# Optimization experiments

Measured on AMD Instinct MI355X. Metric: run time of the kernel, lower is better.

Reference implementation:

```python
import jax, jax.numpy as jnp
import numpy as np

B, N, C_X, D_MODEL, D_OUT, S = 32, 4096, 1, 64, 1, 2
D_IN = C_X + D_MODEL  # 65, channels entering graph_conv


def setup_inputs() -> dict:
    key = jax.random.key(0)
    ks = jax.random.split(key, 8)
    x = jax.random.normal(ks[0], (B, C_X, N), dtype=jnp.float32)
    h = jax.random.normal(ks[1], (B, D_MODEL, N), dtype=jnp.float32)
    # stacked support matrices (fwd/bwd normalized adjacency), used as a list of supports
    adj = jax.random.uniform(ks[2], (S, N, N), dtype=jnp.float32) / N
    # graph_conv.mlp : Conv2d(S*D_IN -> D_MODEL, 1x1)
    W_mlp = jax.random.normal(ks[3], (D_MODEL, S * D_IN), dtype=jnp.float32) / np.sqrt(S * D_IN)
    b_mlp = jnp.zeros((D_MODEL,), jnp.float32)
    # lin_out : Conv1d(2*D_MODEL -> D_MODEL, k=1)
    W_lin = jax.random.normal(ks[4], (D_MODEL, 2 * D_MODEL), dtype=jnp.float32) / np.sqrt(2 * D_MODEL)
    b_lin = jnp.zeros((D_MODEL,), jnp.float32)
    # read_out : Conv1d(2*D_MODEL -> D_OUT, k=1)
    W_read = jax.random.normal(ks[5], (D_OUT, 2 * D_MODEL), dtype=jnp.float32) / np.sqrt(2 * D_MODEL)
    b_read = jnp.zeros((D_OUT,), jnp.float32)
    prelu_a = jnp.array(0.25, jnp.float32)  # nn.PReLU() default: single shared slope
    return {"x": x, "h": h, "adj": adj, "W_mlp": W_mlp, "b_mlp": b_mlp,
            "W_lin": W_lin, "b_lin": b_lin, "W_read": W_read, "b_read": b_read,
            "prelu_a": prelu_a}


def conv1x1(W, b, x):
    # x: [B, C_in, N] -> [B, C_out, N]
    return jnp.einsum('oc,bcn->bon', W, x) + b[None, :, None]


def reference(x, h, adj, W_mlp, b_mlp, W_lin, b_lin, W_read, b_read, prelu_a):
    # x: [B, C_X, N], h: [B, D_MODEL, N], adj: [S, N, N]
    x_in = jnp.concatenate([x, h], axis=1)  # [B, D_IN, N]
    # SpatialConvOrderK (order=1, include_self=False):
    # out[b,c,w] per support s = sum_v x_in[b,c,v] * adj[s,w,v]
    hops = jnp.einsum('bcv,swv->bscw', x_in, adj)  # [B, S, D_IN, N]
    feats = hops.reshape(B, S * D_IN, N)           # channel-cat over supports
    out = conv1x1(W_mlp, b_mlp, feats)             # [B, D_MODEL, N]
    out = jnp.concatenate([out, h], axis=1)        # [B, 2*D_MODEL, N]
    out = conv1x1(W_lin, b_lin, out)               # [B, D_MODEL, N]
    out = jnp.where(out >= 0, out, prelu_a * out)  # PReLU
    out = jnp.concatenate([out, h], axis=1)        # [B, 2*D_MODEL, N]
    return (conv1x1(W_read, b_read, out), out)
```

## Files before the change

kernel.cpp:

```cpp
#include <hip/hip_runtime.h>
#include <cstdint>

#define N_NODES 4096
#define DM 64
#define K_DIM 8192
#define M_DIM 2048

typedef uint8_t u8;
using i32x8   = __attribute__((ext_vector_type(8))) int;
using floatx4 = __attribute__((ext_vector_type(4))) float;

#define GLOAD_LDS16(gp, lp)                                                     \
  __builtin_amdgcn_global_load_lds(                                             \
      reinterpret_cast<const __attribute__((address_space(1))) void*>(          \
          reinterpret_cast<uintptr_t>(gp)),                                     \
      reinterpret_cast<__attribute__((address_space(3))) void*>(                \
          (uint32_t)reinterpret_cast<uintptr_t>(lp)),                           \
      16, 0, 0)

__device__ inline int pk_fp8x4(float f0, float f1, float f2, float f3) {
  int r = __builtin_amdgcn_cvt_pk_fp8_f32(f0, f1, 0, false);
  r     = __builtin_amdgcn_cvt_pk_fp8_f32(f2, f3, r, true);
  return r;
}

__global__ __launch_bounds__(256) void k_prep(const float* __restrict__ adj,
                                              u8* __restrict__ BT8,
                                              const float* __restrict__ x,
                                              const float* __restrict__ h,
                                              const float* __restrict__ Wmlp,
                                              u8* __restrict__ A8) {
  __shared__ __align__(16) float Ws[DM * 68];
  uint32_t bi = blockIdx.x;
  if (bi >= 1024u) {
    const uint32_t lane = threadIdx.x & 63u;
    uint32_t gw = (bi - 1024u) * 4u + (threadIdx.x >> 6);
    for (uint32_t sc = gw; sc < 16384u; sc += 8192u) {
      const float4* src = reinterpret_cast<const float4*>(adj) + (size_t)sc * 512u + lane;
      float4 f[8];
#pragma unroll
      for (int q = 0; q < 8; ++q) f[q] = src[(size_t)q * 64];
      uint32_t row = sc >> 1;
      uint32_t s = row >> 12, w = row & 4095u;
      u8* dst = BT8 + (size_t)w * K_DIM + s * N_NODES + (sc & 1u) * 2048u + lane * 4u;
#pragma unroll
      for (int q = 0; q < 8; ++q) {
        int p = pk_fp8x4(f[q].x * 4096.f, f[q].y * 4096.f, f[q].z * 4096.f, f[q].w * 4096.f);
        *reinterpret_cast<int*>(dst + q * 256) = p;
      }
    }
    return;
  }
  uint32_t b2 = bi;
  uint32_t v0 = (b2 & 15u) * 256u;
  uint32_t s  = (b2 >> 4) & 1u;
  uint32_t b  = b2 >> 5;
  for (uint32_t t = threadIdx.x; t < DM * 68; t += 256) {
    uint32_t d = t / 68u, c = t % 68u;
    Ws[t] = (c < 65u) ? Wmlp[d * 130u + s * 65u + c] : 0.f;
  }
  __syncthreads();

  const uint32_t tv = threadIdx.x & 63u;
  const uint32_t td = threadIdx.x >> 6;
  const uint32_t v  = v0 + tv * 4u;

  float acc[16][4];
#pragma unroll
  for (int d = 0; d < 16; ++d)
#pragma unroll
    for (int k = 0; k < 4; ++k) acc[d][k] = 0.f;

  for (int c0 = 0; c0 < 64; c0 += 4) {
    float4 in4[4];
#pragma unroll
    for (int j = 0; j < 4; ++j) {
      int c = c0 + j;
      const float* src = (c == 0) ? (x + (size_t)b * N_NODES + v)
                                  : (h + ((size_t)b * DM + (c - 1)) * N_NODES + v);
      in4[j] = *reinterpret_cast<const float4*>(src);
    }
#pragma unroll
    for (int d = 0; d < 16; ++d) {
      const float4 w4 = *reinterpret_cast<const float4*>(&Ws[(td * 16 + d) * 68 + c0]);
      acc[d][0] += w4.x * in4[0].x + w4.y * in4[1].x + w4.z * in4[2].x + w4.w * in4[3].x;
      acc[d][1] += w4.x * in4[0].y + w4.y * in4[1].y + w4.z * in4[2].y + w4.w * in4[3].y;
      acc[d][2] += w4.x * in4[0].z + w4.y * in4[1].z + w4.z * in4[2].z + w4.w * in4[3].z;
      acc[d][3] += w4.x * in4[0].w + w4.y * in4[1].w + w4.z * in4[2].w + w4.w * in4[3].w;
    }
  }
  {
    float4 in4 = *reinterpret_cast<const float4*>(h + ((size_t)b * DM + 63) * N_NODES + v);
#pragma unroll
    for (int d = 0; d < 16; ++d) {
      float w = Ws[(td * 16 + d) * 68 + 64];
      acc[d][0] += w * in4.x; acc[d][1] += w * in4.y;
      acc[d][2] += w * in4.z; acc[d][3] += w * in4.w;
    }
  }
#pragma unroll
  for (int d = 0; d < 16; ++d) {
    int p = pk_fp8x4(acc[d][0], acc[d][1], acc[d][2], acc[d][3]);
    *reinterpret_cast<int*>(A8 + (size_t)(b * DM + td * 16 + d) * K_DIM + s * N_NODES + v) = p;
  }
}

__global__ void k_gemm(const u8* __restrict__ A, const u8* __restrict__ BT,
                       const float* __restrict__ h,
                       const float* __restrict__ bmlp, const float* __restrict__ Wlin,
                       const float* __restrict__ blin, const float* __restrict__ Wread,
                       const float* __restrict__ bread, const float* __restrict__ pa,
                       float* __restrict__ out0, float* __restrict__ out1) {
  __shared__ __align__(32) char smem[64 * 132 * 4];
  __shared__ __align__(16) float sbm[DM], sbl[DM], sWr[128];
  __shared__ __align__(16) float psum[8 * 128];

  u8 (*As)[128][32] = reinterpret_cast<u8(*)[128][32]>(smem);
  u8 (*Bs)[128][32] = reinterpret_cast<u8(*)[128][32]>(smem + 16384);
  float (*gco)[132] = reinterpret_cast<float(*)[132]>(smem);

  const int tid  = threadIdx.x;
  const int lane = tid & 63;
  const int wave = tid >> 6;
  const int wr = wave >> 1, wc = wave & 1;

  uint32_t bi  = blockIdx.x;
  uint32_t bi2 = (bi & 7u) * 64u + (bi >> 3);
  const int xt = bi2 & 31, yt = bi2 >> 5;
  const int m0 = yt * 128, n0 = xt * 128;
  const int b0 = yt * 2;

  if (tid < DM)  { sbm[tid] = bmlp[tid]; sbl[tid] = blin[tid]; }
  if (tid < 128) sWr[tid] = Wread[tid];
  const float aP = pa[0];
  const float br = bread[0];

  const int srow  = lane >> 1;
  const int shalf = (lane & 1) * 16;
  const u8* Ag = A  + (size_t)(m0 + wave * 32 + srow) * K_DIM + shalf;
  const u8* Bg = BT + (size_t)(n0 + wave * 32 + srow) * K_DIM + shalf;
  u8* AsB[4]; u8* BsB[4];
#pragma unroll
  for (int q = 0; q < 4; ++q) { AsB[q] = &As[q][wave * 32][0]; BsB[q] = &Bs[q][wave * 32][0]; }

  floatx4 acc[4][4];
#pragma unroll
  for (int i = 0; i < 4; ++i)
#pragma unroll
    for (int j = 0; j < 4; ++j) acc[i][j] = (floatx4){0.f, 0.f, 0.f, 0.f};

  const int fm = lane & 15;
  const int fq = lane >> 4;
  const int SC1 = 0x7F7F7F7F;

  for (int k0 = 0; k0 < 8192; k0 += 128) {
#pragma unroll
    for (int q = 0; q < 4; ++q) GLOAD_LDS16(Ag + k0 + q * 32, AsB[q]);
#pragma unroll
    for (int q = 0; q < 4; ++q) GLOAD_LDS16(Bg + k0 + q * 32, BsB[q]);
    __syncthreads();

    i32x8 af[4], bfr[4];
#pragma unroll
    for (int i = 0; i < 4; ++i)
      af[i] = *reinterpret_cast<const i32x8*>(&As[fq][wr * 64 + i * 16 + fm][0]);
#pragma unroll
    for (int j = 0; j < 4; ++j)
      bfr[j] = *reinterpret_cast<const i32x8*>(&Bs[fq][wc * 64 + j * 16 + fm][0]);
#pragma unroll
    for (int i = 0; i < 4; ++i)
#pragma unroll
      for (int j = 0; j < 4; ++j)
        acc[i][j] = __builtin_amdgcn_mfma_scale_f32_16x16x128_f8f6f4(
            af[i], bfr[j], acc[i][j], 0, 0, 0, SC1, 0, SC1);
    __syncthreads();
  }

  const float KS = 1.0f / 4096.0f;
  const int cr = (lane >> 4) * 4;
  const int cc = lane & 15;
  const int dsub = wave * 2 + (lane >> 5);
  const int ncol = (lane & 31) * 4;
  const float* Wl0 = Wlin + (size_t)(dsub * 8) * 128;

  for (int p = 0; p < 2; ++p) {
    if (wr == p) {
#pragma unroll
      for (int i = 0; i < 4; ++i)
#pragma unroll
        for (int j = 0; j < 4; ++j) {
#pragma unroll
          for (int r = 0; r < 4; ++r) {
            int d = i * 16 + cr + r;
            gco[d][wc * 64 + j * 16 + cc] = acc[i][j][r] * KS + sbm[d];
          }
        }
    }
    __syncthreads();

    const int b = b0 + p;
    float z[8][4];
#pragma unroll
    for (int dd = 0; dd < 8; ++dd) {
      float bl = sbl[dsub * 8 + dd];
#pragma unroll
      for (int k = 0; k < 4; ++k) z[dd][k] = bl;
    }

    for (int k0 = 0; k0 < 64; k0 += 4) {
      float4 g[4];
#pragma unroll
      for (int j = 0; j < 4; ++j)
        g[j] = *reinterpret_cast<const float4*>(&gco[k0 + j][ncol]);
#pragma unroll
      for (int dd = 0; dd < 8; ++dd) {
        const float4 w4 = *reinterpret_cast<const float4*>(Wl0 + (size_t)dd * 128 + k0);
        z[dd][0] += w4.x * g[0].x + w4.y * g[1].x + w4.z * g[2].x + w4.w * g[3].x;
        z[dd][1] += w4.x * g[0].y + w4.y * g[1].y + w4.z * g[2].y + w4.w * g[3].y;
        z[dd][2] += w4.x * g[0].z + w4.y * g[1].z + w4.z * g[2].z + w4.w * g[3].z;
        z[dd][3] += w4.x * g[0].w + w4.y * g[1].w + w4.z * g[2].w + w4.w * g[3].w;
      }
    }

    const float* hb = h + (size_t)b * DM * N_NODES + n0 + ncol;
    float* o1b = out1 + (size_t)b * 128 * N_NODES + n0 + ncol;
    float hs[4] = {0.f, 0.f, 0.f, 0.f};
    for (int k0 = 0; k0 < 64; k0 += 4) {
      float4 hv[4];
#pragma unroll
      for (int j = 0; j < 4; ++j)
        hv[j] = *reinterpret_cast<const float4*>(hb + (size_t)(k0 + j) * N_NODES);
#pragma unroll
      for (int dd = 0; dd < 8; ++dd) {
        const float4 w4 = *reinterpret_cast<const float4*>(Wl0 + (size_t)dd * 128 + 64 + k0);
        z[dd][0] += w4.x * hv[0].x + w4.y * hv[1].x + w4.z * hv[2].x + w4.w * hv[3].x;
        z[dd][1] += w4.x * hv[0].y + w4.y * hv[1].y + w4.z * hv[2].y + w4.w * hv[3].y;
        z[dd][2] += w4.x * hv[0].z + w4.y * hv[1].z + w4.z * hv[2].z + w4.w * hv[3].z;
        z[dd][3] += w4.x * hv[0].w + w4.y * hv[1].w + w4.z * hv[2].w + w4.w * hv[3].w;
      }
      if (dsub == 0) {
#pragma unroll
        for (int j = 0; j < 4; ++j) {
          *reinterpret_cast<float4*>(o1b + (size_t)(64 + k0 + j) * N_NODES) = hv[j];
          float w = sWr[64 + k0 + j];
          hs[0] += w * hv[j].x; hs[1] += w * hv[j].y;
          hs[2] += w * hv[j].z; hs[3] += w * hv[j].w;
        }
      }
    }

    float rp[4] = {0.f, 0.f, 0.f, 0.f};
#pragma unroll
    for (int dd = 0; dd < 8; ++dd) {
      int dp = dsub * 8 + dd;
      float4 o2;
      o2.x = z[dd][0] >= 0.f ? z[dd][0] : aP * z[dd][0];
      o2.y = z[dd][1] >= 0.f ? z[dd][1] : aP * z[dd][1];
      o2.z = z[dd][2] >= 0.f ? z[dd][2] : aP * z[dd][2];
      o2.w = z[dd][3] >= 0.f ? z[dd][3] : aP * z[dd][3];
      *reinterpret_cast<float4*>(o1b + (size_t)dp * N_NODES) = o2;
      float w = sWr[dp];
      rp[0] += w * o2.x; rp[1] += w * o2.y; rp[2] += w * o2.z; rp[3] += w * o2.w;
    }
    if (dsub == 0) {
      rp[0] += hs[0]; rp[1] += hs[1]; rp[2] += hs[2]; rp[3] += hs[3];
    }
    {
      float4 rv; rv.x = rp[0]; rv.y = rp[1]; rv.z = rp[2]; rv.w = rp[3];
      *reinterpret_cast<float4*>(&psum[dsub * 128 + ncol]) = rv;
    }
    __syncthreads();
    if (wave == 0 && lane < 32) {
      float s0[4];
#pragma unroll
      for (int k = 0; k < 4; ++k) {
        float s = br;
#pragma unroll
        for (int ds = 0; ds < 8; ++ds) s += psum[ds * 128 + ncol + k];
        s0[k] = s;
      }
      float4 ov; ov.x = s0[0]; ov.y = s0[1]; ov.z = s0[2]; ov.w = s0[3];
      *reinterpret_cast<float4*>(out0 + (size_t)b * N_NODES + n0 + ncol) = ov;
    }
    __syncthreads();
  }
}

extern "C" void kernel_launch(void* const* d_in, const int* in_sizes, int n_in,
                              void* d_out, int out_size, void* d_ws, size_t ws_size,
                              hipStream_t stream) {
  const float* x     = (const float*)d_in[0];
  const float* h     = (const float*)d_in[1];
  const float* adj   = (const float*)d_in[2];
  const float* Wmlp  = (const float*)d_in[3];
  const float* bmlp  = (const float*)d_in[4];
  const float* Wlin  = (const float*)d_in[5];
  const float* blin  = (const float*)d_in[6];
  const float* Wread = (const float*)d_in[7];
  const float* bread = (const float*)d_in[8];
  const float* pa    = (const float*)d_in[9];

  char* ws = (char*)d_ws;
  u8*    Abuf  = (u8*)ws;
  u8*    BTbuf = (u8*)(ws + (16ull << 20));
  float* out0 = (float*)d_out;
  float* out1 = out0 + 131072;

  hipLaunchKernelGGL(k_prep, dim3(3072), dim3(256), 0, stream,
                     adj, BTbuf, x, h, Wmlp, Abuf);
  hipLaunchKernelGGL(k_gemm, dim3(512),  dim3(256), 0, stream,
                     Abuf, BTbuf, h, bmlp, Wlin, blin, Wread, bread, pa, out0, out1);
}
```

Before: 449.8 us.

## Use 512-thread GEMM blocks with split load roles and XCD-aware tile mapping

```diff
diff --git a/kernel.cpp b/kernel.cpp
--- a/kernel.cpp
+++ b/kernel.cpp
@@ -105,15 +105,16 @@
   }
 }
 
-__global__ void k_gemm(const u8* __restrict__ A, const u8* __restrict__ BT,
-                       const float* __restrict__ h,
-                       const float* __restrict__ bmlp, const float* __restrict__ Wlin,
-                       const float* __restrict__ blin, const float* __restrict__ Wread,
-                       const float* __restrict__ bread, const float* __restrict__ pa,
-                       float* __restrict__ out0, float* __restrict__ out1) {
+__global__ __launch_bounds__(512, 4) void k_gemm(
+    const u8* __restrict__ A, const u8* __restrict__ BT,
+    const float* __restrict__ h,
+    const float* __restrict__ bmlp, const float* __restrict__ Wlin,
+    const float* __restrict__ blin, const float* __restrict__ Wread,
+    const float* __restrict__ bread, const float* __restrict__ pa,
+    float* __restrict__ out0, float* __restrict__ out1) {
   __shared__ __align__(32) char smem[64 * 132 * 4];
   __shared__ __align__(16) float sbm[DM], sbl[DM], sWr[128];
-  __shared__ __align__(16) float psum[8 * 128];
+  __shared__ __align__(16) float psum[16 * 128];
 
   u8 (*As)[128][32] = reinterpret_cast<u8(*)[128][32]>(smem);
   u8 (*Bs)[128][32] = reinterpret_cast<u8(*)[128][32]>(smem + 16384);
@@ -125,27 +126,31 @@
   const int wr = wave >> 1, wc = wave & 1;
 
   uint32_t bi  = blockIdx.x;
-  uint32_t bi2 = (bi & 7u) * 64u + (bi >> 3);
-  const int xt = bi2 & 31, yt = bi2 >> 5;
+  uint32_t xcd = bi & 7u, idx = bi >> 3;
+  const int yt = (int)((xcd & 1u) * 8u + (idx & 7u));
+  const int xt = (int)((xcd >> 1) * 8u + (idx >> 3));
   const int m0 = yt * 128, n0 = xt * 128;
   const int b0 = yt * 2;
 
   if (tid < DM)  { sbm[tid] = bmlp[tid]; sbl[tid] = blin[tid]; }
-  if (tid < 128) sWr[tid] = Wread[tid];
+  if (tid >= 64 && tid < 192) sWr[tid - 64] = Wread[tid - 64];
   const float aP = pa[0];
   const float br = bread[0];
 
   const int srow  = lane >> 1;
   const int shalf = (lane & 1) * 16;
-  const u8* Ag = A  + (size_t)(m0 + wave * 32 + srow) * K_DIM + shalf;
-  const u8* Bg = BT + (size_t)(n0 + wave * 32 + srow) * K_DIM + shalf;
-  u8* AsB[4]; u8* BsB[4];
-#pragma unroll
-  for (int q = 0; q < 4; ++q) { AsB[q] = &As[q][wave * 32][0]; BsB[q] = &Bs[q][wave * 32][0]; }
-
-  floatx4 acc[4][4];
-#pragma unroll
-  for (int i = 0; i < 4; ++i)
+  const bool isA  = wave < 4;
+  const int wrow  = (wave & 3) * 32;
+  const u8* Sg = (isA ? A + (size_t)(m0 + wrow + srow) * K_DIM
+                      : BT + (size_t)(n0 + wrow + srow) * K_DIM) + shalf;
+  u8* SdB[4];
+#pragma unroll
+  for (int q = 0; q < 4; ++q)
+    SdB[q] = isA ? &As[q][wrow][0] : &Bs[q][wrow][0];
+
+  floatx4 acc[2][4];
+#pragma unroll
+  for (int i = 0; i < 2; ++i)
 #pragma unroll
     for (int j = 0; j < 4; ++j) acc[i][j] = (floatx4){0.f, 0.f, 0.f, 0.f};
 
@@ -155,20 +160,18 @@
 
   for (int k0 = 0; k0 < 8192; k0 += 128) {
 #pragma unroll
-    for (int q = 0; q < 4; ++q) GLOAD_LDS16(Ag + k0 + q * 32, AsB[q]);
-#pragma unroll
-    for (int q = 0; q < 4; ++q) GLOAD_LDS16(Bg + k0 + q * 32, BsB[q]);
-    __syncthreads();
-
-    i32x8 af[4], bfr[4];
-#pragma unroll
-    for (int i = 0; i < 4; ++i)
-      af[i] = *reinterpret_cast<const i32x8*>(&As[fq][wr * 64 + i * 16 + fm][0]);
+    for (int q = 0; q < 4; ++q) GLOAD_LDS16(Sg + k0 + q * 32, SdB[q]);
+    __syncthreads();
+
+    i32x8 af[2], bfr[4];
+#pragma unroll
+    for (int i = 0; i < 2; ++i)
+      af[i] = *reinterpret_cast<const i32x8*>(&As[fq][wr * 32 + i * 16 + fm][0]);
 #pragma unroll
     for (int j = 0; j < 4; ++j)
       bfr[j] = *reinterpret_cast<const i32x8*>(&Bs[fq][wc * 64 + j * 16 + fm][0]);
 #pragma unroll
-    for (int i = 0; i < 4; ++i)
+    for (int i = 0; i < 2; ++i)
 #pragma unroll
       for (int j = 0; j < 4; ++j)
         acc[i][j] = __builtin_amdgcn_mfma_scale_f32_16x16x128_f8f6f4(
@@ -179,19 +182,19 @@
   const float KS = 1.0f / 4096.0f;
   const int cr = (lane >> 4) * 4;
   const int cc = lane & 15;
-  const int dsub = wave * 2 + (lane >> 5);
-  const int ncol = (lane & 31) * 4;
-  const float* Wl0 = Wlin + (size_t)(dsub * 8) * 128;
+  const int dsub = tid >> 5;
+  const int ncol = (tid & 31) * 4;
+  const float* Wl0 = Wlin + (size_t)(dsub * 4) * 128;
 
   for (int p = 0; p < 2; ++p) {
-    if (wr == p) {
-#pragma unroll
-      for (int i = 0; i < 4; ++i)
+    if ((wr >> 1) == p) {
+#pragma unroll
+      for (int i = 0; i < 2; ++i)
 #pragma unroll
         for (int j = 0; j < 4; ++j) {
 #pragma unroll
           for (int r = 0; r < 4; ++r) {
-            int d = i * 16 + cr + r;
+            int d = (wr & 1) * 32 + i * 16 + cr + r;
             gco[d][wc * 64 + j * 16 + cc] = acc[i][j][r] * KS + sbm[d];
           }
         }
@@ -199,10 +202,10 @@
     __syncthreads();
 
     const int b = b0 + p;
-    float z[8][4];
-#pragma unroll
-    for (int dd = 0; dd < 8; ++dd) {
-      float bl = sbl[dsub * 8 + dd];
+    float z[4][4];
+#pragma unroll
+    for (int dd = 0; dd < 4; ++dd) {
+      float bl = sbl[dsub * 4 + dd];
 #pragma unroll
       for (int k = 0; k < 4; ++k) z[dd][k] = bl;
     }
@@ -213,7 +216,7 @@
       for (int j = 0; j < 4; ++j)
         g[j] = *reinterpret_cast<const float4*>(&gco[k0 + j][ncol]);
 #pragma unroll
-      for (int dd = 0; dd < 8; ++dd) {
+      for (int dd = 0; dd < 4; ++dd) {
         const float4 w4 = *reinterpret_cast<const float4*>(Wl0 + (size_t)dd * 128 + k0);
         z[dd][0] += w4.x * g[0].x + w4.y * g[1].x + w4.z * g[2].x + w4.w * g[3].x;
         z[dd][1] += w4.x * g[0].y + w4.y * g[1].y + w4.z * g[2].y + w4.w * g[3].y;
@@ -231,7 +234,7 @@
       for (int j = 0; j < 4; ++j)
         hv[j] = *reinterpret_cast<const float4*>(hb + (size_t)(k0 + j) * N_NODES);
 #pragma unroll
-      for (int dd = 0; dd < 8; ++dd) {
+      for (int dd = 0; dd < 4; ++dd) {
         const float4 w4 = *reinterpret_cast<const float4*>(Wl0 + (size_t)dd * 128 + 64 + k0);
         z[dd][0] += w4.x * hv[0].x + w4.y * hv[1].x + w4.z * hv[2].x + w4.w * hv[3].x;
         z[dd][1] += w4.x * hv[0].y + w4.y * hv[1].y + w4.z * hv[2].y + w4.w * hv[3].y;
@@ -251,8 +254,8 @@
 
     float rp[4] = {0.f, 0.f, 0.f, 0.f};
 #pragma unroll
-    for (int dd = 0; dd < 8; ++dd) {
-      int dp = dsub * 8 + dd;
+    for (int dd = 0; dd < 4; ++dd) {
+      int dp = dsub * 4 + dd;
       float4 o2;
       o2.x = z[dd][0] >= 0.f ? z[dd][0] : aP * z[dd][0];
       o2.y = z[dd][1] >= 0.f ? z[dd][1] : aP * z[dd][1];
@@ -270,13 +273,13 @@
       *reinterpret_cast<float4*>(&psum[dsub * 128 + ncol]) = rv;
     }
     __syncthreads();
-    if (wave == 0 && lane < 32) {
+    if (tid < 32) {
       float s0[4];
 #pragma unroll
       for (int k = 0; k < 4; ++k) {
         float s = br;
 #pragma unroll
-        for (int ds = 0; ds < 8; ++ds) s += psum[ds * 128 + ncol + k];
+        for (int ds = 0; ds < 16; ++ds) s += psum[ds * 128 + ncol + k];
         s0[k] = s;
       }
       float4 ov; ov.x = s0[0]; ov.y = s0[1]; ov.z = s0[2]; ov.w = s0[3];
@@ -308,6 +311,6 @@
 
   hipLaunchKernelGGL(k_prep, dim3(3072), dim3(256), 0, stream,
                      adj, BTbuf, x, h, Wmlp, Abuf);
-  hipLaunchKernelGGL(k_gemm, dim3(512),  dim3(256), 0, stream,
+  hipLaunchKernelGGL(k_gemm, dim3(512),  dim3(512), 0, stream,
                      Abuf, BTbuf, h, bmlp, Wlin, blin, Wread, bread, pa, out0, out1);
 }
```

Measured after the change: 975.5 us. +116.9%, slower.

## Load FP8 MFMA fragments directly from global into registers with double buffering

Applied to the files above, without the earlier changes.

```diff
diff --git a/kernel.cpp b/kernel.cpp
--- a/kernel.cpp
+++ b/kernel.cpp
@@ -9,14 +9,6 @@
 typedef uint8_t u8;
 using i32x8   = __attribute__((ext_vector_type(8))) int;
 using floatx4 = __attribute__((ext_vector_type(4))) float;
-
-#define GLOAD_LDS16(gp, lp)                                                     \
-  __builtin_amdgcn_global_load_lds(                                             \
-      reinterpret_cast<const __attribute__((address_space(1))) void*>(          \
-          reinterpret_cast<uintptr_t>(gp)),                                     \
-      reinterpret_cast<__attribute__((address_space(3))) void*>(                \
-          (uint32_t)reinterpret_cast<uintptr_t>(lp)),                           \
-      16, 0, 0)
 
 __device__ inline int pk_fp8x4(float f0, float f1, float f2, float f3) {
   int r = __builtin_amdgcn_cvt_pk_fp8_f32(f0, f1, 0, false);
@@ -105,19 +97,17 @@
   }
 }
 
-__global__ void k_gemm(const u8* __restrict__ A, const u8* __restrict__ BT,
-                       const float* __restrict__ h,
-                       const float* __restrict__ bmlp, const float* __restrict__ Wlin,
-                       const float* __restrict__ blin, const float* __restrict__ Wread,
-                       const float* __restrict__ bread, const float* __restrict__ pa,
-                       float* __restrict__ out0, float* __restrict__ out1) {
-  __shared__ __align__(32) char smem[64 * 132 * 4];
+__global__ __launch_bounds__(256, 2) void k_gemm(
+    const u8* __restrict__ A, const u8* __restrict__ BT,
+    const float* __restrict__ h,
+    const float* __restrict__ bmlp, const float* __restrict__ Wlin,
+    const float* __restrict__ blin, const float* __restrict__ Wread,
+    const float* __restrict__ bread, const float* __restrict__ pa,
+    float* __restrict__ out0, float* __restrict__ out1) {
+  __shared__ __align__(16) float gco[64][132];
+  __shared__ __align__(16) float sW[DM * 132];
   __shared__ __align__(16) float sbm[DM], sbl[DM], sWr[128];
   __shared__ __align__(16) float psum[8 * 128];
-
-  u8 (*As)[128][32] = reinterpret_cast<u8(*)[128][32]>(smem);
-  u8 (*Bs)[128][32] = reinterpret_cast<u8(*)[128][32]>(smem + 16384);
-  float (*gco)[132] = reinterpret_cast<float(*)[132]>(smem);
 
   const int tid  = threadIdx.x;
   const int lane = tid & 63;
@@ -130,58 +120,72 @@
   const int m0 = yt * 128, n0 = xt * 128;
   const int b0 = yt * 2;
 
+  for (int t = tid; t < DM * 128; t += 256) {
+    int d = t >> 7, c = t & 127;
+    sW[d * 132 + c] = Wlin[t];
+  }
   if (tid < DM)  { sbm[tid] = bmlp[tid]; sbl[tid] = blin[tid]; }
   if (tid < 128) sWr[tid] = Wread[tid];
   const float aP = pa[0];
   const float br = bread[0];
 
-  const int srow  = lane >> 1;
-  const int shalf = (lane & 1) * 16;
-  const u8* Ag = A  + (size_t)(m0 + wave * 32 + srow) * K_DIM + shalf;
-  const u8* Bg = BT + (size_t)(n0 + wave * 32 + srow) * K_DIM + shalf;
-  u8* AsB[4]; u8* BsB[4];
-#pragma unroll
-  for (int q = 0; q < 4; ++q) { AsB[q] = &As[q][wave * 32][0]; BsB[q] = &Bs[q][wave * 32][0]; }
-
-  floatx4 acc[4][4];
-#pragma unroll
-  for (int i = 0; i < 4; ++i)
-#pragma unroll
-    for (int j = 0; j < 4; ++j) acc[i][j] = (floatx4){0.f, 0.f, 0.f, 0.f};
-
   const int fm = lane & 15;
   const int fq = lane >> 4;
+  const u8* Ab = A  + (size_t)(m0 + wr * 64 + fm) * K_DIM + fq * 32;
+  const u8* Bb = BT + (size_t)(n0 + wc * 64 + fm) * K_DIM + fq * 32;
+
+  floatx4 acc[4][4];
+#pragma unroll
+  for (int i = 0; i < 4; ++i)
+#pragma unroll
+    for (int j = 0; j < 4; ++j) acc[i][j] = (floatx4){0.f, 0.f, 0.f, 0.f};
+
   const int SC1 = 0x7F7F7F7F;
 
-  for (int k0 = 0; k0 < 8192; k0 += 128) {
-#pragma unroll
-    for (int q = 0; q < 4; ++q) GLOAD_LDS16(Ag + k0 + q * 32, AsB[q]);
-#pragma unroll
-    for (int q = 0; q < 4; ++q) GLOAD_LDS16(Bg + k0 + q * 32, BsB[q]);
-    __syncthreads();
-
-    i32x8 af[4], bfr[4];
+  i32x8 a0[4], b0v[4], a1[4], b1[4];
+#pragma unroll
+  for (int i = 0; i < 4; ++i)
+    a0[i] = *reinterpret_cast<const i32x8*>(Ab + (size_t)i * 16 * K_DIM);
+#pragma unroll
+  for (int j = 0; j < 4; ++j)
+    b0v[j] = *reinterpret_cast<const i32x8*>(Bb + (size_t)j * 16 * K_DIM);
+
+  for (int k0 = 0; k0 < 8192; k0 += 256) {
 #pragma unroll
     for (int i = 0; i < 4; ++i)
-      af[i] = *reinterpret_cast<const i32x8*>(&As[fq][wr * 64 + i * 16 + fm][0]);
+      a1[i] = *reinterpret_cast<const i32x8*>(Ab + (size_t)i * 16 * K_DIM + k0 + 128);
 #pragma unroll
     for (int j = 0; j < 4; ++j)
-      bfr[j] = *reinterpret_cast<const i32x8*>(&Bs[fq][wc * 64 + j * 16 + fm][0]);
+      b1[j] = *reinterpret_cast<const i32x8*>(Bb + (size_t)j * 16 * K_DIM + k0 + 128);
 #pragma unroll
     for (int i = 0; i < 4; ++i)
 #pragma unroll
       for (int j = 0; j < 4; ++j)
         acc[i][j] = __builtin_amdgcn_mfma_scale_f32_16x16x128_f8f6f4(
-            af[i], bfr[j], acc[i][j], 0, 0, 0, SC1, 0, SC1);
-    __syncthreads();
-  }
+            a0[i], b0v[j], acc[i][j], 0, 0, 0, SC1, 0, SC1);
+    if (k0 + 256 < 8192) {
+#pragma unroll
+      for (int i = 0; i < 4; ++i)
+        a0[i] = *reinterpret_cast<const i32x8*>(Ab + (size_t)i * 16 * K_DIM + k0 + 256);
+#pragma unroll
+      for (int j = 0; j < 4; ++j)
+        b0v[j] = *reinterpret_cast<const i32x8*>(Bb + (size_t)j * 16 * K_DIM + k0 + 256);
+    }
+#pragma unroll
+    for (int i = 0; i < 4; ++i)
+#pragma unroll
+      for (int j = 0; j < 4; ++j)
+        acc[i][j] = __builtin_amdgcn_mfma_scale_f32_16x16x128_f8f6f4(
+            a1[i], b1[j], acc[i][j], 0, 0, 0, SC1, 0, SC1);
+  }
+
+  __syncthreads();
 
   const float KS = 1.0f / 4096.0f;
   const int cr = (lane >> 4) * 4;
   const int cc = lane & 15;
   const int dsub = wave * 2 + (lane >> 5);
   const int ncol = (lane & 31) * 4;
-  const float* Wl0 = Wlin + (size_t)(dsub * 8) * 128;
 
   for (int p = 0; p < 2; ++p) {
     if (wr == p) {
@@ -214,7 +218,7 @@
         g[j] = *reinterpret_cast<const float4*>(&gco[k0 + j][ncol]);
 #pragma unroll
       for (int dd = 0; dd < 8; ++dd) {
-        const float4 w4 = *reinterpret_cast<const float4*>(Wl0 + (size_t)dd * 128 + k0);
+        const float4 w4 = *reinterpret_cast<const float4*>(&sW[(dsub * 8 + dd) * 132 + k0]);
         z[dd][0] += w4.x * g[0].x + w4.y * g[1].x + w4.z * g[2].x + w4.w * g[3].x;
         z[dd][1] += w4.x * g[0].y + w4.y * g[1].y + w4.z * g[2].y + w4.w * g[3].y;
         z[dd][2] += w4.x * g[0].z + w4.y * g[1].z + w4.z * g[2].z + w4.w * g[3].z;
@@ -232,7 +236,7 @@
         hv[j] = *reinterpret_cast<const float4*>(hb + (size_t)(k0 + j) * N_NODES);
 #pragma unroll
       for (int dd = 0; dd < 8; ++dd) {
-        const float4 w4 = *reinterpret_cast<const float4*>(Wl0 + (size_t)dd * 128 + 64 + k0);
+        const float4 w4 = *reinterpret_cast<const float4*>(&sW[(dsub * 8 + dd) * 132 + 64 + k0]);
         z[dd][0] += w4.x * hv[0].x + w4.y * hv[1].x + w4.z * hv[2].x + w4.w * hv[3].x;
         z[dd][1] += w4.x * hv[0].y + w4.y * hv[1].y + w4.z * hv[2].y + w4.w * hv[3].y;
         z[dd][2] += w4.x * hv[0].z + w4.y * hv[1].z + w4.z * hv[2].z + w4.w * hv[3].z;
```

New measurement: 915.4 us. 2.04x slower.

## Double-buffer LDS tiles in FP8 GEMM to overlap global loads with MFMA

Applied to the files above, without the earlier changes.

```diff
diff --git a/kernel.cpp b/kernel.cpp
--- a/kernel.cpp
+++ b/kernel.cpp
@@ -105,19 +105,16 @@
   }
 }
 
-__global__ void k_gemm(const u8* __restrict__ A, const u8* __restrict__ BT,
-                       const float* __restrict__ h,
-                       const float* __restrict__ bmlp, const float* __restrict__ Wlin,
-                       const float* __restrict__ blin, const float* __restrict__ Wread,
-                       const float* __restrict__ bread, const float* __restrict__ pa,
-                       float* __restrict__ out0, float* __restrict__ out1) {
-  __shared__ __align__(32) char smem[64 * 132 * 4];
+__global__ __launch_bounds__(256) void k_gemm(
+    const u8* __restrict__ A, const u8* __restrict__ BT,
+    const float* __restrict__ h,
+    const float* __restrict__ bmlp, const float* __restrict__ Wlin,
+    const float* __restrict__ blin, const float* __restrict__ Wread,
+    const float* __restrict__ bread, const float* __restrict__ pa,
+    float* __restrict__ out0, float* __restrict__ out1) {
+  __shared__ __align__(32) u8 smem[2][32768];
   __shared__ __align__(16) float sbm[DM], sbl[DM], sWr[128];
   __shared__ __align__(16) float psum[8 * 128];
-
-  u8 (*As)[128][32] = reinterpret_cast<u8(*)[128][32]>(smem);
-  u8 (*Bs)[128][32] = reinterpret_cast<u8(*)[128][32]>(smem + 16384);
-  float (*gco)[132] = reinterpret_cast<float(*)[132]>(smem);
 
   const int tid  = threadIdx.x;
   const int lane = tid & 63;
@@ -139,9 +136,16 @@
   const int shalf = (lane & 1) * 16;
   const u8* Ag = A  + (size_t)(m0 + wave * 32 + srow) * K_DIM + shalf;
   const u8* Bg = BT + (size_t)(n0 + wave * 32 + srow) * K_DIM + shalf;
-  u8* AsB[4]; u8* BsB[4];
-#pragma unroll
-  for (int q = 0; q < 4; ++q) { AsB[q] = &As[q][wave * 32][0]; BsB[q] = &Bs[q][wave * 32][0]; }
+
+#define STAGE(buf, koff)                                                        \
+  {                                                                             \
+    _Pragma("unroll")                                                           \
+    for (int q = 0; q < 4; ++q) {                                               \
+      GLOAD_LDS16(Ag + (koff) + q * 32, &smem[buf][q * 4096 + wave * 1024]);    \
+      GLOAD_LDS16(Bg + (koff) + q * 32,                                         \
+                  &smem[buf][16384 + q * 4096 + wave * 1024]);                  \
+    }                                                                           \
+  }
 
   floatx4 acc[4][4];
 #pragma unroll
@@ -153,29 +157,35 @@
   const int fq = lane >> 4;
   const int SC1 = 0x7F7F7F7F;
 
+  STAGE(0, 0);
+  __syncthreads();
+  int cur = 0;
+
   for (int k0 = 0; k0 < 8192; k0 += 128) {
-#pragma unroll
-    for (int q = 0; q < 4; ++q) GLOAD_LDS16(Ag + k0 + q * 32, AsB[q]);
-#pragma unroll
-    for (int q = 0; q < 4; ++q) GLOAD_LDS16(Bg + k0 + q * 32, BsB[q]);
-    __syncthreads();
+    if (k0 + 128 < 8192) STAGE(cur ^ 1, k0 + 128);
 
     i32x8 af[4], bfr[4];
+    const u8* Ab = &smem[cur][fq * 4096];
+    const u8* Bb = &smem[cur][16384 + fq * 4096];
 #pragma unroll
     for (int i = 0; i < 4; ++i)
-      af[i] = *reinterpret_cast<const i32x8*>(&As[fq][wr * 64 + i * 16 + fm][0]);
+      af[i] = *reinterpret_cast<const i32x8*>(Ab + (wr * 64 + i * 16 + fm) * 32);
 #pragma unroll
     for (int j = 0; j < 4; ++j)
-      bfr[j] = *reinterpret_cast<const i32x8*>(&Bs[fq][wc * 64 + j * 16 + fm][0]);
+      bfr[j] = *reinterpret_cast<const i32x8*>(Bb + (wc * 64 + j * 16 + fm) * 32);
 #pragma unroll
     for (int i = 0; i < 4; ++i)
 #pragma unroll
       for (int j = 0; j < 4; ++j)
         acc[i][j] = __builtin_amdgcn_mfma_scale_f32_16x16x128_f8f6f4(
             af[i], bfr[j], acc[i][j], 0, 0, 0, SC1, 0, SC1);
+
     __syncthreads();
-  }
-
+    cur ^= 1;
+  }
+#undef STAGE
+
+  float (*gco)[132] = reinterpret_cast<float(*)[132]>(&smem[0][0]);
   const float KS = 1.0f / 4096.0f;
   const int cr = (lane >> 4) * 4;
   const int cc = lane & 15;
```

New measurement: 522.0 us. 16.0% more time.
